# Kernel tuning notes

Hardware: AMD Instinct MI355X
Metric: run time of the kernel (lower is better)

## Reference

```python
import jax, jax.numpy as jnp
import numpy as np

LATENT = 2000
N_GROUPS = 10000  # loci_count // window_size
KERNEL = 20       # window_size * 2; per-group input length is 1 so out length == KERNEL
BATCH = 128
EPS = 1e-5
SLOPE = 0.1


def setup_inputs() -> dict:
    key = jax.random.key(0)
    k1, k2, k3, k4, k5 = jax.random.split(key, 5)
    return {
        "z": jax.random.normal(k1, (BATCH, LATENT), dtype=jnp.float32),
        "W_fc": jax.random.normal(k2, (N_GROUPS, LATENT), dtype=jnp.float32) * 0.02,
        "b_fc": jax.random.normal(k3, (N_GROUPS,), dtype=jnp.float32) * 0.02,
        "gamma": jnp.ones((N_GROUPS,), dtype=jnp.float32),
        "beta": jnp.zeros((N_GROUPS,), dtype=jnp.float32),
        "conv_w": jax.random.normal(k4, (N_GROUPS, KERNEL), dtype=jnp.float32) * 0.1,
        "conv_b": jax.random.normal(k5, (N_GROUPS,), dtype=jnp.float32) * 0.02,
    }


def reference(z, W_fc, b_fc, gamma, beta, conv_w, conv_b):
    # Linear: (B, L) @ (L, G) -> (B, G)
    h = jnp.einsum("bl,gl->bg", z, W_fc) + b_fc
    # BatchNorm1d (training mode: biased batch statistics, eps=1e-5)
    mean = jnp.mean(h, axis=0)
    var = jnp.mean(jnp.square(h - mean), axis=0)
    h = (h - mean) * jax.lax.rsqrt(var + EPS) * gamma + beta
    h = jnp.where(h >= 0, h, SLOPE * h)  # LeakyReLU(0.1)
    # Grouped ConvTranspose1d with per-group input length 1 degenerates to
    # an outer product per channel: y[b,g,k] = h[b,g]*w[g,k] + b[g]
    y = h[:, :, None] * conv_w[None, :, :] + conv_b[None, :, None]  # (B, G, K)
    y = jnp.where(y >= 0, y, SLOPE * y)  # LeakyReLU(0.1)
    out = jax.nn.sigmoid(y.reshape(z.shape[0], N_GROUPS * KERNEL))
    return out
```

## Files before the change

kernel.cpp:

```cpp
#include <hip/hip_runtime.h>
#include <hip/hip_bf16.h>
#include <stdint.h>

#define BATCH 128
#define LAT   2000
#define NG    10000
#define KW    20
#define OUTW  (NG * KW)
#define EPSV  1e-5f

#define NKT   32
#define EG    16
#define WPAD  2056
#define HR_STRIDE 132

typedef __bf16 bf16x8 __attribute__((ext_vector_type(8)));
typedef float  f32x4  __attribute__((ext_vector_type(4)));

__device__ __forceinline__ ushort f2bf(float f) {
  uint32_t u = __builtin_bit_cast(uint32_t, f);
  u = (u + 0x7FFFu + ((u >> 16) & 1u)) >> 16;
  return (ushort)u;
}

__device__ __forceinline__ int4 pack8(const float* p) {
  float4 f0 = *(const float4*)p;
  float4 f1 = *(const float4*)(p + 4);
  int4 v;
  v.x = (int)((uint32_t)f2bf(f0.x) | ((uint32_t)f2bf(f0.y) << 16));
  v.y = (int)((uint32_t)f2bf(f0.z) | ((uint32_t)f2bf(f0.w) << 16));
  v.z = (int)((uint32_t)f2bf(f1.x) | ((uint32_t)f2bf(f1.y) << 16));
  v.w = (int)((uint32_t)f2bf(f1.z) | ((uint32_t)f2bf(f1.w) << 16));
  return v;
}

__global__ __launch_bounds__(256) void zprep_kernel(
    const float* __restrict__ zp, int4* __restrict__ zlin) {
  const int cg = blockIdx.x * 256 + threadIdx.x;
  const int r  = cg >> 8;
  const int ck = cg & 255;
  const int k0 = ck * 8;
  int4 v = make_int4(0, 0, 0, 0);
  if (k0 < LAT) v = pack8(zp + (size_t)r * LAT + k0);
  const int kt = ck >> 3, kk = (ck >> 2) & 1, q = ck & 3;
  const int dst = ((kt * 2 + kk) * 8 + (r >> 4)) * 64 + q * 16 + (r & 15);
  zlin[dst] = v;
}

__global__ __launch_bounds__(1024, 4) void fused16_kernel(
    const int4* __restrict__ zlin, const float* __restrict__ wp,
    const float* __restrict__ gammap, const float* __restrict__ betap,
    const float* __restrict__ convwp, const float* __restrict__ convbp,
    float* __restrict__ out) {
  const int tid = threadIdx.x;
  const int g0  = blockIdx.x * EG;

  __shared__ __attribute__((aligned(16))) ushort Wl[EG * WPAD];
  __shared__ float  h_raw[EG * HR_STRIDE];
  __shared__ float4 cw_s[EG * 5];
  __shared__ float  cb_s[EG];
  __shared__ float  scale_s[EG];
  __shared__ float  shift_s[EG];

  if (tid < EG * 5)
    cw_s[tid] = *(const float4*)(convwp + (size_t)g0 * KW + tid * 4);
  if (tid < EG) cb_s[tid] = convbp[g0 + tid];

#pragma unroll
  for (int i = 0; i < 4; ++i) {
    int cc  = i * 1024 + tid;
    int row = cc >> 8;
    int c   = cc & 255;
    int kt  = c >> 3, j = c & 7;
    int k0  = kt * 64 + j * 8;
    int4 v  = make_int4(0, 0, 0, 0);
    if (k0 < LAT) v = pack8(wp + (size_t)(g0 + row) * LAT + k0);
    *(int4*)&Wl[row * WPAD + kt * 64 + j * 8] = v;
  }

  const int lane = tid & 63;
  const int w    = tid >> 6;
  const int wg   = w & 7;
  const int half = w >> 3;
  const int q    = lane >> 4;
  const int cl   = lane & 15;
  const int rb   = wg * 16 + cl;
  const int t0   = half * 16;

  const int4* zw = zlin + (size_t)wg * 64 + lane;
  const ushort* wl = &Wl[cl * WPAD];

  f32x4 acc = {0.f, 0.f, 0.f, 0.f};

  int4 za0 = zw[(t0 * 2 + 0) * 512], za1 = zw[(t0 * 2 + 1) * 512];
  int4 zb0 = zw[(t0 * 2 + 2) * 512], zb1 = zw[(t0 * 2 + 3) * 512];
  int4 zc0 = zw[(t0 * 2 + 4) * 512], zc1 = zw[(t0 * 2 + 5) * 512];
  int4 zd0 = zw[(t0 * 2 + 6) * 512], zd1 = zw[(t0 * 2 + 7) * 512];

  __syncthreads();

#pragma unroll 4
  for (int i = 0; i < 16; ++i) {
    const int t  = t0 + i;
    const int tp = (i + 4 < 16) ? (t + 4) : t;
    int4 ne0 = zw[(tp * 2 + 0) * 512];
    int4 ne1 = zw[(tp * 2 + 1) * 512];

    bf16x8 a0 = *(const bf16x8*)&wl[t * 64 + q * 8];
    bf16x8 a1 = *(const bf16x8*)&wl[t * 64 + (4 + q) * 8];

    acc = __builtin_amdgcn_mfma_f32_16x16x32_bf16(
        a0, __builtin_bit_cast(bf16x8, za0), acc, 0, 0, 0);
    acc = __builtin_amdgcn_mfma_f32_16x16x32_bf16(
        a1, __builtin_bit_cast(bf16x8, za1), acc, 0, 0, 0);

    za0 = zb0; za1 = zb1;
    zb0 = zc0; zb1 = zc1;
    zc0 = zd0; zc1 = zd1;
    zd0 = ne0; zd1 = ne1;
  }

  if (half == 0) {
#pragma unroll
    for (int r = 0; r < 4; ++r)
      h_raw[(q * 4 + r) * HR_STRIDE + rb] = acc[r];
  }
  __syncthreads();
  if (half == 1) {
#pragma unroll
    for (int r = 0; r < 4; ++r)
      h_raw[(q * 4 + r) * HR_STRIDE + rb] += acc[r];
  }
  __syncthreads();

  {
    const int gw = w;
    const int l  = lane;
    const float2 a = *(const float2*)&h_raw[gw * HR_STRIDE + l * 2];
    float sm = a.x + a.y;
    float sq = a.x * a.x + a.y * a.y;
#pragma unroll
    for (int m = 1; m < 64; m <<= 1) {
      sm += __shfl_xor(sm, m);
      sq += __shfl_xor(sq, m);
    }
    if (l == 0) {
      float mean = sm * (1.f / 128.f);
      float var  = sq * (1.f / 128.f) - mean * mean;
      var = (var < 0.f) ? 0.f : var;
      float inv   = __builtin_amdgcn_rsqf(var + EPSV);
      float scale = inv * gammap[g0 + gw];
      scale_s[gw] = scale;
      shift_s[gw] = betap[g0 + gw] - mean * scale;
    }
  }
  __syncthreads();

  if (tid < 960) {
    const int col4 = tid % 80;
    const int r0   = tid / 80;
    const int gl   = col4 / 5;
    const float4 w4  = cw_s[col4];
    const float  cb  = cb_s[gl];
    const float  scl = scale_s[gl];
    const float  sft = shift_s[gl];
    const float* hsrc = &h_raw[gl * HR_STRIDE];
    float* obase = out + (size_t)g0 * KW + (size_t)col4 * 4;
    for (int j = 0; j < 11; ++j) {
      const int row = j * 12 + r0;
      if (row < BATCH) {
        float h = hsrc[row];
        h = fmaf(h, scl, sft);
        h = fmaxf(h, h * 0.1f);
        float y0 = fmaf(h, w4.x, cb);
        float y1 = fmaf(h, w4.y, cb);
        float y2 = fmaf(h, w4.z, cb);
        float y3 = fmaf(h, w4.w, cb);
        y0 = fmaxf(y0, y0 * 0.1f);
        y1 = fmaxf(y1, y1 * 0.1f);
        y2 = fmaxf(y2, y2 * 0.1f);
        y3 = fmaxf(y3, y3 * 0.1f);
        float4 ov;
        ov.x = __builtin_amdgcn_rcpf(1.f + exp2f(y0 * -1.44269504f));
        ov.y = __builtin_amdgcn_rcpf(1.f + exp2f(y1 * -1.44269504f));
        ov.z = __builtin_amdgcn_rcpf(1.f + exp2f(y2 * -1.44269504f));
        ov.w = __builtin_amdgcn_rcpf(1.f + exp2f(y3 * -1.44269504f));
        *(float4*)(obase + (size_t)row * OUTW) = ov;
      }
    }
  }
}

#define BKF 64
__global__ __launch_bounds__(256, 2) void fused_decoder_kernel(
    const float* __restrict__ zp, const float* __restrict__ wp,
    const float* __restrict__ gammap, const float* __restrict__ betap,
    const float* __restrict__ convwp, const float* __restrict__ convbp,
    float* __restrict__ out) {
  const int tid = threadIdx.x;
  const int g0  = blockIdx.x * 32;

  __shared__ ushort As[BATCH * BKF];
  __shared__ ushort Bs[32 * BKF];
  __shared__ float statS[2][2][16];
  __shared__ float statQ[2][2][16];

  const int lane = tid & 63;
  const int w    = tid >> 6;
  const int wm   = w & 1;
  const int wn   = w >> 1;
  const int q    = lane >> 4;
  const int cl   = lane & 15;

  f32x4 acc[4];
  const f32x4 vzero = {0.f, 0.f, 0.f, 0.f};
#pragma unroll
  for (int i = 0; i < 4; ++i) acc[i] = vzero;

  for (int it = 0; it < 32; ++it) {
    const int k0 = it * BKF;
    __syncthreads();
#pragma unroll
    for (int i = 0; i < 4; ++i) {
      int c = i * 256 + tid;
      int r = c >> 3, sc = c & 7;
      int gk = k0 + sc * 8;
      int4 v = make_int4(0, 0, 0, 0);
      if (gk < LAT) v = pack8(zp + (size_t)r * LAT + gk);
      *(int4*)&As[r * BKF + ((sc ^ (r & 7)) << 3)] = v;
    }
    {
      int r = tid >> 3, sc = tid & 7;
      int g  = g0 + r;
      int gk = k0 + sc * 8;
      int4 v = make_int4(0, 0, 0, 0);
      if (gk < LAT && g < NG) v = pack8(wp + (size_t)g * LAT + gk);
      *(int4*)&Bs[r * BKF + ((sc ^ (r & 7)) << 3)] = v;
    }
    __syncthreads();
#pragma unroll
    for (int kk = 0; kk < 2; ++kk) {
      int sc = kk * 4 + q;
      bf16x8 af[4], bfr;
#pragma unroll
      for (int mt = 0; mt < 4; ++mt) {
        int ra = wm * 64 + mt * 16 + cl;
        af[mt] = *(const bf16x8*)&As[ra * BKF + ((sc ^ (ra & 7)) << 3)];
      }
      {
        int rbx = wn * 16 + cl;
        bfr = *(const bf16x8*)&Bs[rbx * BKF + ((sc ^ (rbx & 7)) << 3)];
      }
#pragma unroll
      for (int mt = 0; mt < 4; ++mt)
        acc[mt] = __builtin_amdgcn_mfma_f32_16x16x32_bf16(af[mt], bfr,
                                                          acc[mt], 0, 0, 0);
    }
  }

  float s = 0.f, ss = 0.f;
#pragma unroll
  for (int mt = 0; mt < 4; ++mt)
#pragma unroll
    for (int r = 0; r < 4; ++r) {
      float v = acc[mt][r];
      s += v; ss += v * v;
    }
  s += __shfl_xor(s, 16); ss += __shfl_xor(ss, 16);
  s += __shfl_xor(s, 32); ss += __shfl_xor(ss, 32);
  if (q == 0) { statS[wm][wn][cl] = s; statQ[wm][wn][cl] = ss; }
  __syncthreads();

  const int gcol = g0 + wn * 16 + cl;
  const int gc   = (gcol < NG) ? gcol : (NG - 1);
  float S = statS[0][wn][cl] + statS[1][wn][cl];
  float Q = statQ[0][wn][cl] + statQ[1][wn][cl];
  float mean = S * (1.f / 128.f);
  float var  = Q * (1.f / 128.f) - mean * mean;
  var = (var < 0.f) ? 0.f : var;
  float inv = __builtin_amdgcn_rsqf(var + EPSV);
  float ga = gammap[gc], be = betap[gc], cb = convbp[gc];
  float wv[KW];
  {
    const float4* pw = (const float4*)(convwp + (size_t)gc * KW);
#pragma unroll
    for (int j = 0; j < 5; ++j) {
      float4 f = pw[j];
      wv[4 * j] = f.x; wv[4 * j + 1] = f.y;
      wv[4 * j + 2] = f.z; wv[4 * j + 3] = f.w;
    }
  }
  float scale = inv * ga;
  float shift = be - mean * scale;
  const bool ok = (gcol < NG);
#pragma unroll
  for (int mt = 0; mt < 4; ++mt) {
#pragma unroll
    for (int r = 0; r < 4; ++r) {
      float h = acc[mt][r] * scale + shift;
      h = fmaxf(h, h * 0.1f);
      int b = wm * 64 + mt * 16 + q * 4 + r;
      float4 ov[5];
#pragma unroll
      for (int j = 0; j < 5; ++j) {
        float y0 = h * wv[4 * j]     + cb;
        float y1 = h * wv[4 * j + 1] + cb;
        float y2 = h * wv[4 * j + 2] + cb;
        float y3 = h * wv[4 * j + 3] + cb;
        y0 = fmaxf(y0, y0 * 0.1f);
        y1 = fmaxf(y1, y1 * 0.1f);
        y2 = fmaxf(y2, y2 * 0.1f);
        y3 = fmaxf(y3, y3 * 0.1f);
        ov[j].x = __builtin_amdgcn_rcpf(1.f + exp2f(y0 * -1.44269504f));
        ov[j].y = __builtin_amdgcn_rcpf(1.f + exp2f(y1 * -1.44269504f));
        ov[j].z = __builtin_amdgcn_rcpf(1.f + exp2f(y2 * -1.44269504f));
        ov[j].w = __builtin_amdgcn_rcpf(1.f + exp2f(y3 * -1.44269504f));
      }
      if (ok) {
        float4* po = (float4*)(out + (size_t)b * OUTW + (size_t)gcol * KW);
#pragma unroll
        for (int j = 0; j < 5; ++j) po[j] = ov[j];
      }
    }
  }
}

extern "C" void kernel_launch(void* const* d_in, const int* in_sizes, int n_in,
                              void* d_out, int out_size, void* d_ws, size_t ws_size,
                              hipStream_t stream) {
  const float* z     = (const float*)d_in[0];
  const float* W     = (const float*)d_in[1];
  const float* gamma = (const float*)d_in[3];
  const float* beta  = (const float*)d_in[4];
  const float* convw = (const float*)d_in[5];
  const float* convb = (const float*)d_in[6];
  float* out = (float*)d_out;

  const size_t zlin_bytes = (size_t)BATCH * 256 * 16;

  if (ws_size >= zlin_bytes) {
    int4* zlin = (int4*)d_ws;
    zprep_kernel<<<128, 256, 0, stream>>>(z, zlin);
    fused16_kernel<<<NG / EG, 1024, 0, stream>>>(zlin, W, gamma, beta,
                                                 convw, convb, out);
  } else {
    fused_decoder_kernel<<<(NG + 31) / 32, 256, 0, stream>>>(
        z, W, gamma, beta, convw, convb, out);
  }
}
```

Before: 201.6 us.

## Process 80 groups per block with double-buffered, swizzled W staging in LDS

Each block now handles 80 groups instead of 16, so the z operand loaded per K-step feeds five MFMA tiles rather than one. The whole W slice is no longer staged up front; 64-wide K chunks are streamed through a double-buffered, XOR-swizzled LDS buffer, and the next chunk is loaded while the current one is multiplied. This is meant to cut redundant z traffic and hide W load latency behind MFMA work. In exchange the grid shrinks from 625 to 125 blocks, which may underfill the GPU's compute units, and there is now a barrier on every K-step.

```diff
diff --git a/kernel.cpp b/kernel.cpp
--- a/kernel.cpp
+++ b/kernel.cpp
@@ -10,8 +10,7 @@
 #define EPSV  1e-5f
 
 #define NKT   32
-#define EG    16
-#define WPAD  2056
+#define EG    80
 #define HR_STRIDE 132
 
 typedef __bf16 bf16x8 __attribute__((ext_vector_type(8)));
@@ -32,6 +31,13 @@
   v.z = (int)((uint32_t)f2bf(f1.x) | ((uint32_t)f2bf(f1.y) << 16));
   v.w = (int)((uint32_t)f2bf(f1.z) | ((uint32_t)f2bf(f1.w) << 16));
   return v;
+}
+
+__device__ __forceinline__ bf16x8 cvt8(float4 a, float4 b) {
+  bf16x8 r;
+  r[0] = (__bf16)a.x; r[1] = (__bf16)a.y; r[2] = (__bf16)a.z; r[3] = (__bf16)a.w;
+  r[4] = (__bf16)b.x; r[5] = (__bf16)b.y; r[6] = (__bf16)b.z; r[7] = (__bf16)b.w;
+  return r;
 }
 
 __global__ __launch_bounds__(256) void zprep_kernel(
@@ -47,7 +53,7 @@
   zlin[dst] = v;
 }
 
-__global__ __launch_bounds__(1024, 4) void fused16_kernel(
+__global__ __launch_bounds__(1024, 4) void fused80_kernel(
     const int4* __restrict__ zlin, const float* __restrict__ wp,
     const float* __restrict__ gammap, const float* __restrict__ betap,
     const float* __restrict__ convwp, const float* __restrict__ convbp,
@@ -55,7 +61,7 @@
   const int tid = threadIdx.x;
   const int g0  = blockIdx.x * EG;
 
-  __shared__ __attribute__((aligned(16))) ushort Wl[EG * WPAD];
+  __shared__ __attribute__((aligned(16))) ushort Wt[4 * 5120];
   __shared__ float  h_raw[EG * HR_STRIDE];
   __shared__ float4 cw_s[EG * 5];
   __shared__ float  cb_s[EG];
@@ -65,18 +71,6 @@
   if (tid < EG * 5)
     cw_s[tid] = *(const float4*)(convwp + (size_t)g0 * KW + tid * 4);
   if (tid < EG) cb_s[tid] = convbp[g0 + tid];
-
-#pragma unroll
-  for (int i = 0; i < 4; ++i) {
-    int cc  = i * 1024 + tid;
-    int row = cc >> 8;
-    int c   = cc & 255;
-    int kt  = c >> 3, j = c & 7;
-    int k0  = kt * 64 + j * 8;
-    int4 v  = make_int4(0, 0, 0, 0);
-    if (k0 < LAT) v = pack8(wp + (size_t)(g0 + row) * LAT + k0);
-    *(int4*)&Wl[row * WPAD + kt * 64 + j * 8] = v;
-  }
 
   const int lane = tid & 63;
   const int w    = tid >> 6;
@@ -88,55 +82,108 @@
   const int t0   = half * 16;
 
   const int4* zw = zlin + (size_t)wg * 64 + lane;
-  const ushort* wl = &Wl[cl * WPAD];
-
-  f32x4 acc = {0.f, 0.f, 0.f, 0.f};
-
-  int4 za0 = zw[(t0 * 2 + 0) * 512], za1 = zw[(t0 * 2 + 1) * 512];
-  int4 zb0 = zw[(t0 * 2 + 2) * 512], zb1 = zw[(t0 * 2 + 3) * 512];
-  int4 zc0 = zw[(t0 * 2 + 4) * 512], zc1 = zw[(t0 * 2 + 5) * 512];
-  int4 zd0 = zw[(t0 * 2 + 6) * 512], zd1 = zw[(t0 * 2 + 7) * 512];
-
-  __syncthreads();
-
-#pragma unroll 4
-  for (int i = 0; i < 16; ++i) {
-    const int t  = t0 + i;
-    const int tp = (i + 4 < 16) ? (t + 4) : t;
-    int4 ne0 = zw[(tp * 2 + 0) * 512];
-    int4 ne1 = zw[(tp * 2 + 1) * 512];
-
-    bf16x8 a0 = *(const bf16x8*)&wl[t * 64 + q * 8];
-    bf16x8 a1 = *(const bf16x8*)&wl[t * 64 + (4 + q) * 8];
-
-    acc = __builtin_amdgcn_mfma_f32_16x16x32_bf16(
-        a0, __builtin_bit_cast(bf16x8, za0), acc, 0, 0, 0);
-    acc = __builtin_amdgcn_mfma_f32_16x16x32_bf16(
-        a1, __builtin_bit_cast(bf16x8, za1), acc, 0, 0, 0);
-
-    za0 = zb0; za1 = zb1;
-    zb0 = zc0; zb1 = zc1;
-    zc0 = zd0; zc1 = zd1;
-    zd0 = ne0; zd1 = ne1;
+
+  const int c0h  = (tid >= 640);
+  const int c0r  = (tid - c0h * 640) >> 3;
+  const int c0j  = tid & 7;
+  const float* c0p = wp + (size_t)(g0 + c0r) * LAT;
+  const int c0kb = c0h * 1024 + c0j * 8;
+  const int inner0 = c0h * 5120 + c0r * 64 + ((c0j ^ (c0r & 7)) << 3);
+  const int c1r  = (384 + tid) >> 3;
+  const int c1j  = tid & 7;
+  const float* c1p = wp + (size_t)(g0 + c1r) * LAT;
+  const int c1kb = 1024 + c1j * 8;
+  const int inner1 = 5120 + c1r * 64 + ((c1j ^ (c1r & 7)) << 3);
+
+  const int a0off = half * 5120 + cl * 64 + ((q       ^ (cl & 7)) << 3);
+  const int a1off = half * 5120 + cl * 64 + (((4 + q) ^ (cl & 7)) << 3);
+
+  f32x4 acc[5];
+  const f32x4 vzero = {0.f, 0.f, 0.f, 0.f};
+#pragma unroll
+  for (int i = 0; i < 5; ++i) acc[i] = vzero;
+  const float4 fz4 = make_float4(0.f, 0.f, 0.f, 0.f);
+
+  float4 P0 = fz4, P1 = fz4, P2 = fz4, P3 = fz4;
+  {
+    int k0 = c0kb;
+    if (k0 < LAT) { P0 = *(const float4*)(c0p + k0);
+                    P1 = *(const float4*)(c0p + k0 + 4); }
+    if (tid < 256) {
+      int k1 = c1kb;
+      if (k1 < LAT) { P2 = *(const float4*)(c1p + k1);
+                      P3 = *(const float4*)(c1p + k1 + 4); }
+    }
+  }
+  int4 za0 = zw[(size_t)(t0 * 2 + 0) * 512], za1 = zw[(size_t)(t0 * 2 + 1) * 512];
+  int4 zb0 = zw[(size_t)(t0 * 2 + 2) * 512], zb1 = zw[(size_t)(t0 * 2 + 3) * 512];
+  *(bf16x8*)&Wt[inner0] = cvt8(P0, P1);
+  if (tid < 256) *(bf16x8*)&Wt[inner1] = cvt8(P2, P3);
+  __syncthreads();
+
+#pragma unroll 2
+  for (int it = 0; it < 16; ++it) {
+    const int cbuf = it & 1, nbuf = cbuf ^ 1;
+
+    float4 Q0 = fz4, Q1 = fz4, Q2 = fz4, Q3 = fz4;
+    if (it < 15) {
+      int k0 = c0kb + (it + 1) * 64;
+      if (k0 < LAT) { Q0 = *(const float4*)(c0p + k0);
+                      Q1 = *(const float4*)(c0p + k0 + 4); }
+      if (tid < 256) {
+        int k1 = c1kb + (it + 1) * 64;
+        if (k1 < LAT) { Q2 = *(const float4*)(c1p + k1);
+                        Q3 = *(const float4*)(c1p + k1 + 4); }
+      }
+    }
+    const int i2 = (it + 2 < 16) ? (it + 2) : it;
+    int4 nz0 = zw[(size_t)((t0 + i2) * 2 + 0) * 512];
+    int4 nz1 = zw[(size_t)((t0 + i2) * 2 + 1) * 512];
+
+    {
+      const ushort* wb = &Wt[cbuf * 10240];
+#pragma unroll
+      for (int mt = 0; mt < 5; ++mt) {
+        bf16x8 a = *(const bf16x8*)&wb[a0off + mt * 1024];
+        acc[mt] = __builtin_amdgcn_mfma_f32_16x16x32_bf16(
+            a, __builtin_bit_cast(bf16x8, za0), acc[mt], 0, 0, 0);
+      }
+#pragma unroll
+      for (int mt = 0; mt < 5; ++mt) {
+        bf16x8 a = *(const bf16x8*)&wb[a1off + mt * 1024];
+        acc[mt] = __builtin_amdgcn_mfma_f32_16x16x32_bf16(
+            a, __builtin_bit_cast(bf16x8, za1), acc[mt], 0, 0, 0);
+      }
+    }
+    if (it < 15) {
+      *(bf16x8*)&Wt[nbuf * 10240 + inner0] = cvt8(Q0, Q1);
+      if (tid < 256) *(bf16x8*)&Wt[nbuf * 10240 + inner1] = cvt8(Q2, Q3);
+    }
+    __syncthreads();
+    za0 = zb0; za1 = zb1; zb0 = nz0; zb1 = nz1;
   }
 
   if (half == 0) {
 #pragma unroll
-    for (int r = 0; r < 4; ++r)
-      h_raw[(q * 4 + r) * HR_STRIDE + rb] = acc[r];
+    for (int mt = 0; mt < 5; ++mt)
+#pragma unroll
+      for (int r = 0; r < 4; ++r)
+        h_raw[(mt * 16 + q * 4 + r) * HR_STRIDE + rb] = acc[mt][r];
   }
   __syncthreads();
   if (half == 1) {
 #pragma unroll
-    for (int r = 0; r < 4; ++r)
-      h_raw[(q * 4 + r) * HR_STRIDE + rb] += acc[r];
-  }
-  __syncthreads();
-
-  {
-    const int gw = w;
-    const int l  = lane;
-    const float2 a = *(const float2*)&h_raw[gw * HR_STRIDE + l * 2];
+    for (int mt = 0; mt < 5; ++mt)
+#pragma unroll
+      for (int r = 0; r < 4; ++r)
+        h_raw[(mt * 16 + q * 4 + r) * HR_STRIDE + rb] += acc[mt][r];
+  }
+  __syncthreads();
+
+#pragma unroll
+  for (int s = 0; s < 5; ++s) {
+    const int g = w * 5 + s;
+    const float2 a = *(const float2*)&h_raw[g * HR_STRIDE + lane * 2];
     float sm = a.x + a.y;
     float sq = a.x * a.x + a.y * a.y;
 #pragma unroll
@@ -144,49 +191,48 @@
       sm += __shfl_xor(sm, m);
       sq += __shfl_xor(sq, m);
     }
-    if (l == 0) {
+    if (lane == 0) {
       float mean = sm * (1.f / 128.f);
       float var  = sq * (1.f / 128.f) - mean * mean;
       var = (var < 0.f) ? 0.f : var;
       float inv   = __builtin_amdgcn_rsqf(var + EPSV);
-      float scale = inv * gammap[g0 + gw];
-      scale_s[gw] = scale;
-      shift_s[gw] = betap[g0 + gw] - mean * scale;
-    }
-  }
-  __syncthreads();
-
-  if (tid < 960) {
-    const int col4 = tid % 80;
-    const int r0   = tid / 80;
+      float scale = inv * gammap[g0 + g];
+      scale_s[g] = scale;
+      shift_s[g] = betap[g0 + g] - mean * scale;
+    }
+  }
+  __syncthreads();
+
+  if (tid < 800) {
+    const int col4 = tid % 400;
+    const int r0   = tid / 400;
     const int gl   = col4 / 5;
     const float4 w4  = cw_s[col4];
-    const float  cb  = cb_s[gl];
+    const float  cbv = cb_s[gl];
     const float  scl = scale_s[gl];
     const float  sft = shift_s[gl];
     const float* hsrc = &h_raw[gl * HR_STRIDE];
     float* obase = out + (size_t)g0 * KW + (size_t)col4 * 4;
-    for (int j = 0; j < 11; ++j) {
-      const int row = j * 12 + r0;
-      if (row < BATCH) {
-        float h = hsrc[row];
-        h = fmaf(h, scl, sft);
-        h = fmaxf(h, h * 0.1f);
-        float y0 = fmaf(h, w4.x, cb);
-        float y1 = fmaf(h, w4.y, cb);
-        float y2 = fmaf(h, w4.z, cb);
-        float y3 = fmaf(h, w4.w, cb);
-        y0 = fmaxf(y0, y0 * 0.1f);
-        y1 = fmaxf(y1, y1 * 0.1f);
-        y2 = fmaxf(y2, y2 * 0.1f);
-        y3 = fmaxf(y3, y3 * 0.1f);
-        float4 ov;
-        ov.x = __builtin_amdgcn_rcpf(1.f + exp2f(y0 * -1.44269504f));
-        ov.y = __builtin_amdgcn_rcpf(1.f + exp2f(y1 * -1.44269504f));
-        ov.z = __builtin_amdgcn_rcpf(1.f + exp2f(y2 * -1.44269504f));
-        ov.w = __builtin_amdgcn_rcpf(1.f + exp2f(y3 * -1.44269504f));
-        *(float4*)(obase + (size_t)row * OUTW) = ov;
-      }
+#pragma unroll 2
+    for (int jj = 0; jj < 64; ++jj) {
+      const int row = jj * 2 + r0;
+      float h = hsrc[row];
+      h = fmaf(h, scl, sft);
+      h = fmaxf(h, h * 0.1f);
+      float y0 = fmaf(h, w4.x, cbv);
+      float y1 = fmaf(h, w4.y, cbv);
+      float y2 = fmaf(h, w4.z, cbv);
+      float y3 = fmaf(h, w4.w, cbv);
+      y0 = fmaxf(y0, y0 * 0.1f);
+      y1 = fmaxf(y1, y1 * 0.1f);
+      y2 = fmaxf(y2, y2 * 0.1f);
+      y3 = fmaxf(y3, y3 * 0.1f);
+      float4 ov;
+      ov.x = __builtin_amdgcn_rcpf(1.f + exp2f(y0 * -1.44269504f));
+      ov.y = __builtin_amdgcn_rcpf(1.f + exp2f(y1 * -1.44269504f));
+      ov.z = __builtin_amdgcn_rcpf(1.f + exp2f(y2 * -1.44269504f));
+      ov.w = __builtin_amdgcn_rcpf(1.f + exp2f(y3 * -1.44269504f));
+      *(float4*)(obase + (size_t)row * OUTW) = ov;
     }
   }
 }
@@ -341,7 +387,7 @@
   if (ws_size >= zlin_bytes) {
     int4* zlin = (int4*)d_ws;
     zprep_kernel<<<128, 256, 0, stream>>>(z, zlin);
-    fused16_kernel<<<NG / EG, 1024, 0, stream>>>(zlin, W, gamma, beta,
+    fused80_kernel<<<NG / EG, 1024, 0, stream>>>(zlin, W, gamma, beta,
                                                  convw, convb, out);
   } else {
     fused_decoder_kernel<<<(NG + 31) / 32, 256, 0, stream>>>(
```

Result: slower. 209.0 us (+3.7%).
